# Kernel tuning notes

Measured on AMD Instinct MI355X. Metric: run time of the kernel, lower is better.

## Reference

```python
import jax, jax.numpy as jnp
import numpy as np

B, N, M, D = 2, 2048, 32, 128
H, DH = 8, 16
DI = H * DH            # dim_inner = 128
S = 5                  # 1 + max_degree + max_degree, max_degree = 2
DMLP = 256             # int(2.0 * dim_inner)


def _ln(x, g):  # LayerNorm(bias=False)
    mu = x.mean(-1, keepdims=True)
    var = ((x - mu) ** 2).mean(-1, keepdims=True)
    return (x - mu) / jnp.sqrt(var + 1e-5) * g


def _softclamp(t, v=50.0):
    return jnp.tanh(t / v) * v


def _gather(a, idx):  # a: [b, n, ...], idx: [b, i, j] -> [b, i, j, ...]
    return jax.vmap(lambda t, ix: jnp.take(t, ix, axis=0))(a, idx)


def setup_inputs():
    key = jax.random.key(0)
    ks = jax.random.split(key, 24)
    w = lambda k, i, o: jax.random.normal(k, (i, o), jnp.float32) / np.sqrt(i)
    return {
        'h': jax.random.normal(ks[0], (B, N, D), jnp.float32),
        't_ij': jax.random.normal(ks[1], (B, N, M, D), jnp.float32),
        'r_ij_1': jax.random.normal(ks[2], (B, N, M, 3), jnp.float32),
        'r_ij_2': jax.random.normal(ks[3], (B, N, M, 5), jnp.float32),
        'x_1': jax.random.normal(ks[4], (B, N, D, 3), jnp.float32),
        'x_2': jax.random.normal(ks[5], (B, N, D, 5), jnp.float32),
        'g_hi': jnp.ones((D,), jnp.float32),
        'g_hj': jnp.ones((D,), jnp.float32),
        'Wq': w(ks[6], D, DI),
        'Wk': w(ks[7], D, DI),
        'Wv1': w(ks[8], D, DMLP), 'bv1': jnp.zeros((DMLP,), jnp.float32),
        'Wv2': w(ks[9], DMLP, S * DI), 'bv2': jnp.zeros((S * DI,), jnp.float32),
        'Wp1': w(ks[10], D, DMLP), 'bp1': jnp.zeros((DMLP,), jnp.float32),
        'Wp2': w(ks[11], DMLP, S * DI), 'bp2': jnp.zeros((S * DI,), jnp.float32),
        'Wek': w(ks[12], D, S * DI),
        'Wev': w(ks[13], D, S * DI),
        'Wg': w(ks[14], D, H * S), 'bg': jnp.zeros((H * S,), jnp.float32),
        'Wc': w(ks[15], DI, D),
        'neighbor_indices': jax.random.randint(ks[16], (B, N, M), 0, N),
        'neighbor_mask': jnp.ones((B, N, M), bool),
    }


def reference(h, t_ij, r_ij_1, r_ij_2, x_1, x_2, g_hi, g_hj, Wq, Wk, Wv1, bv1,
              Wv2, bv2, Wp1, bp1, Wp2, bp2, Wek, Wev, Wg, bg, Wc,
              neighbor_indices, neighbor_mask):
    b, n, m = neighbor_indices.shape
    hi = _ln(h, g_hi)
    hj = _ln(h, g_hj)
    q = (hi @ Wq).reshape(b, n, H, DH).transpose(0, 2, 1, 3)               # b h i dh
    k = hj @ Wk                                                            # b n (h dh)
    v = jax.nn.silu(hj @ Wv1 + bv1) @ Wv2 + bv2                            # b n (s h dh)
    pav = jax.nn.silu(hj @ Wp1 + bp1) @ Wp2 + bp2                          # post-attn h values
    ek = jax.nn.silu(t_ij @ Wek)                                           # b i j (s h dh)
    ev = t_ij @ Wev
    # neighbor gathers over the node axis
    k_g = _gather(k, neighbor_indices)                                     # b i j (h dh)
    v_g = _gather(v, neighbor_indices)                                     # b i j (s h dh)
    pav_g = _gather(pav, neighbor_indices)
    heads4 = lambda t: t.reshape(b, n, m, H, DH).transpose(0, 3, 1, 2, 4)          # b h i j dh
    heads5 = lambda t: t.reshape(b, n, m, S, H, DH).transpose(0, 4, 1, 2, 3, 5)    # b h i j s dh
    keys = heads4(k_g)[..., None, :] * heads5(ek)                          # edge-fused keys
    sim = _softclamp(jnp.einsum('bhid,bhijsd->bhijs', q, keys))
    sim = jnp.where(neighbor_mask[:, None, :, :, None], sim, -jnp.finfo(sim.dtype).max)
    attn = jax.nn.softmax(sim, axis=-2)                                    # softmax over neighbors j
    sea = attn[..., None] * heads5(v_g) + heads5(ev) * heads5(pav_g)       # b h i j s dh
    gates = jax.nn.sigmoid(hi @ Wg + bg).reshape(b, n, H, S)               # layout (h s)
    sea = sea * gates.transpose(0, 2, 1, 3)[:, :, :, None, :, None]        # b h i 1 s 1
    out = sea.transpose(0, 2, 3, 4, 1, 5).reshape(b, n, m, S, DI) @ Wc     # b i j s d
    h_res = out[..., 0, :].sum(axis=2)                                     # sum over neighbors
    x_res = []
    for li, (r_l, x_l) in enumerate(((r_ij_1, x_1), (r_ij_2, x_2))):
        r_part = jnp.einsum('bijm,bijd->bidm', r_l, out[..., 1 + li, :])
        xg = _gather(x_l, neighbor_indices)                                # b i j d ml
        x_res.append(r_part + jnp.einsum('bijdm,bijd->bidm', xg, out[..., 3 + li, :]))
    return (h_res, x_res[0], x_res[1])
```

## Files before the change

kernel.cpp:

```cpp
#include <hip/hip_runtime.h>
#include <hip/hip_bf16.h>
#include <cstdint>


typedef __bf16 bf16x8 __attribute__((ext_vector_type(8)));
typedef float  f32x4  __attribute__((ext_vector_type(4)));
typedef unsigned short u16;
typedef unsigned int   u32;

__device__ __forceinline__ float sigm_(float x){ return 1.f/(1.f+__expf(-x)); }
__device__ __forceinline__ float silu_(float x){ return x/(1.f+__expf(-x)); }
__device__ __forceinline__ u16 f2b(float f){
    union{float f; u32 u;} x; x.f = f;
    u32 r = x.u + 0x7FFFu + ((x.u>>16)&1u);
    return (u16)(r>>16);
}
__device__ __forceinline__ float b2f(u16 b){
    union{u32 u; float f;} x; x.u = ((u32)b)<<16; return x.f;
}
union VecU { uint4 u; bf16x8 v; u16 s[8]; };
union Vec4 { uint2 u; u16 s[4]; };
__device__ __forceinline__ bf16x8 ld8(const u16* p){ VecU x; x.u = *(const uint4*)p; return x.v; }

__global__ __launch_bounds__(256) void prep_kernel(
    const float* __restrict__ Wek, const float* __restrict__ Wev,
    const float* __restrict__ Wc,
    const float* __restrict__ x1, const float* __restrict__ x2,
    u16* __restrict__ wekT, u16* __restrict__ wevT, u16* __restrict__ wcT,
    float* __restrict__ xT1, float* __restrict__ xT2, int do_xt)
{
    const int idx = blockIdx.x*256 + threadIdx.x;
    if (idx < 81920) {
        const int n = idx >> 7, k = idx & 127;
        wekT[idx] = f2b(Wek[k*640 + n]);
        wevT[idx] = f2b(Wev[k*640 + n]);
    }
    if (idx < 16384) {
        const int d = idx >> 7, c = idx & 127;
        wcT[idx] = f2b(Wc[c*128 + d]);
    }
    if (do_xt) {
        if (idx < 4096*384) {
            const int node = idx/384, rem = idx%384, m = rem>>7, d = rem&127;
            xT1[idx] = x1[((size_t)node*128 + d)*3 + m];
        }
        if (idx < 4096*640) {
            const int node = idx/640, rem = idx%640, m = rem>>7, d = rem&127;
            xT2[idx] = x2[((size_t)node*128 + d)*5 + m];
        }
    }
}

__global__ __launch_bounds__(256) void node_kernel(
    const float* __restrict__ h,
    const float* __restrict__ g_hi, const float* __restrict__ g_hj,
    const float* __restrict__ Wq, const float* __restrict__ Wk,
    const float* __restrict__ Wv1, const float* __restrict__ bv1,
    const float* __restrict__ Wv2, const float* __restrict__ bv2,
    const float* __restrict__ Wp1, const float* __restrict__ bp1,
    const float* __restrict__ Wp2, const float* __restrict__ bp2,
    const float* __restrict__ Wg, const float* __restrict__ bg,
    float* __restrict__ qws, float* __restrict__ kws,
    float* __restrict__ vpws, float* __restrict__ gws)
{
    const int tid  = threadIdx.x;
    const int base = blockIdx.x * 8;
    __shared__ __align__(16) float hi_s[8][128];
    __shared__ __align__(16) float hj_s[8][128];
    __shared__ __align__(16) float u_s[8][256];

    {
        const int wv = tid >> 6, lane = tid & 63;
        for (int r = wv; r < 8; r += 4) {
            const int node = base + r;
            float a  = h[node*128 + lane];
            float b2 = h[node*128 + 64 + lane];
            float s = a + b2;
            #pragma unroll
            for (int off = 32; off > 0; off >>= 1) s += __shfl_down(s, off);
            s = __shfl(s, 0);
            const float mu = s * (1.f/128.f);
            const float da = a - mu, db = b2 - mu;
            float v = da*da + db*db;
            #pragma unroll
            for (int off = 32; off > 0; off >>= 1) v += __shfl_down(v, off);
            v = __shfl(v, 0);
            const float rstd = rsqrtf(v*(1.f/128.f) + 1e-5f);
            hi_s[r][lane]    = da*rstd*g_hi[lane];
            hi_s[r][64+lane] = db*rstd*g_hi[64+lane];
            hj_s[r][lane]    = da*rstd*g_hj[lane];
            hj_s[r][64+lane] = db*rstd*g_hj[64+lane];
        }
    }
    __syncthreads();

    {
        const int o  = tid & 127;
        const int r0 = (tid >> 7) * 4;
        float aq[4], ak[4];
        #pragma unroll
        for (int r=0;r<4;r++){ aq[r]=0.f; ak[r]=0.f; }
        for (int c0=0;c0<128;c0+=4) {
            float wq0=Wq[(c0+0)*128+o], wq1=Wq[(c0+1)*128+o], wq2=Wq[(c0+2)*128+o], wq3=Wq[(c0+3)*128+o];
            float wk0=Wk[(c0+0)*128+o], wk1=Wk[(c0+1)*128+o], wk2=Wk[(c0+2)*128+o], wk3=Wk[(c0+3)*128+o];
            #pragma unroll
            for (int r=0;r<4;r++) {
                float4 hi4 = *(const float4*)(&hi_s[r0+r][c0]);
                float4 hj4 = *(const float4*)(&hj_s[r0+r][c0]);
                aq[r] += hi4.x*wq0; aq[r] += hi4.y*wq1; aq[r] += hi4.z*wq2; aq[r] += hi4.w*wq3;
                ak[r] += hj4.x*wk0; ak[r] += hj4.y*wk1; ak[r] += hj4.z*wk2; ak[r] += hj4.w*wk3;
            }
        }
        #pragma unroll
        for (int r=0;r<4;r++) {
            qws[(size_t)(base+r0+r)*128 + o] = aq[r];
            kws[(size_t)(base+r0+r)*128 + o] = ak[r];
        }
    }

    {
        const int o = tid;
        float acc[8];
        const float bias = bv1[o];
        #pragma unroll
        for (int r=0;r<8;r++) acc[r]=bias;
        for (int c0=0;c0<128;c0+=4) {
            float w0=Wv1[(c0+0)*256+o], w1=Wv1[(c0+1)*256+o], w2=Wv1[(c0+2)*256+o], w3=Wv1[(c0+3)*256+o];
            #pragma unroll
            for (int r=0;r<8;r++) {
                float4 u4 = *(const float4*)(&hj_s[r][c0]);
                acc[r] += u4.x*w0; acc[r] += u4.y*w1; acc[r] += u4.z*w2; acc[r] += u4.w*w3;
            }
        }
        #pragma unroll
        for (int r=0;r<8;r++) u_s[r][o] = silu_(acc[r]);
    }
    __syncthreads();

    for (int o=tid; o<640; o+=256) {
        float acc[8];
        const float bias = bv2[o];
        #pragma unroll
        for (int r=0;r<8;r++) acc[r]=bias;
        for (int c0=0;c0<256;c0+=4) {
            float w0=Wv2[(c0+0)*640+o], w1=Wv2[(c0+1)*640+o], w2=Wv2[(c0+2)*640+o], w3=Wv2[(c0+3)*640+o];
            #pragma unroll
            for (int r=0;r<8;r++) {
                float4 u4 = *(const float4*)(&u_s[r][c0]);
                acc[r] += u4.x*w0; acc[r] += u4.y*w1; acc[r] += u4.z*w2; acc[r] += u4.w*w3;
            }
        }
        #pragma unroll
        for (int r=0;r<8;r++)
            vpws[(size_t)(base+r)*1280 + (o>>2)*8 + (o&3)] = acc[r];
    }
    __syncthreads();

    {
        const int o = tid;
        float acc[8];
        const float bias = bp1[o];
        #pragma unroll
        for (int r=0;r<8;r++) acc[r]=bias;
        for (int c0=0;c0<128;c0+=4) {
            float w0=Wp1[(c0+0)*256+o], w1=Wp1[(c0+1)*256+o], w2=Wp1[(c0+2)*256+o], w3=Wp1[(c0+3)*256+o];
            #pragma unroll
            for (int r=0;r<8;r++) {
                float4 u4 = *(const float4*)(&hj_s[r][c0]);
                acc[r] += u4.x*w0; acc[r] += u4.y*w1; acc[r] += u4.z*w2; acc[r] += u4.w*w3;
            }
        }
        #pragma unroll
        for (int r=0;r<8;r++) u_s[r][o] = silu_(acc[r]);
    }
    __syncthreads();

    for (int o=tid; o<640; o+=256) {
        float acc[8];
        const float bias = bp2[o];
        #pragma unroll
        for (int r=0;r<8;r++) acc[r]=bias;
        for (int c0=0;c0<256;c0+=4) {
            float w0=Wp2[(c0+0)*640+o], w1=Wp2[(c0+1)*640+o], w2=Wp2[(c0+2)*640+o], w3=Wp2[(c0+3)*640+o];
            #pragma unroll
            for (int r=0;r<8;r++) {
                float4 u4 = *(const float4*)(&u_s[r][c0]);
                acc[r] += u4.x*w0; acc[r] += u4.y*w1; acc[r] += u4.z*w2; acc[r] += u4.w*w3;
            }
        }
        #pragma unroll
        for (int r=0;r<8;r++)
            vpws[(size_t)(base+r)*1280 + (o>>2)*8 + 4 + (o&3)] = acc[r];
    }

    for (int idx=tid; idx<8*40; idx+=256) {
        const int r = idx/40, hs = idx%40;
        float s = bg[hs];
        for (int c=0;c<128;c++) s += hi_s[r][c]*Wg[c*40+hs];
        gws[(size_t)(base+r)*40 + hs] = sigm_(s);
    }
}

template<bool XT>
__global__ __launch_bounds__(512,4) void edge_kernel(
    const float* __restrict__ t_ij,
    const float* __restrict__ r1, const float* __restrict__ r2,
    const float* __restrict__ x1, const float* __restrict__ x2,
    const float* __restrict__ xT1, const float* __restrict__ xT2,
    const u16* __restrict__ wekT, const u16* __restrict__ wevT,
    const u16* __restrict__ wcT,
    const int* __restrict__ nidx,
    const float* __restrict__ qws, const float* __restrict__ kws,
    const float* __restrict__ vpws,
    const float* __restrict__ gws,
    float* __restrict__ out)
{
    const int node = blockIdx.x;
    const int bN   = (node >> 11) << 11;
    const int tid  = threadIdx.x;
    const int grp  = tid >> 8;
    const int ltid = tid & 255;
    const int lane = ltid & 63, w = ltid >> 6;
    const int ll   = lane & 15, lh = lane >> 4;

    __shared__ __align__(16) u16   tj_s[32*128];
    __shared__ __align__(16) u16   chunk_s[2][80*128];
    __shared__ float sim_s[32][40];
    __shared__ __align__(16) float q_s[128];
    __shared__ float g_s[40];
    __shared__ int   jn_s[32];

    u16* chunk = chunk_s[grp];

    if (tid < 32) jn_s[tid] = nidx[node*32 + tid];
    else if (tid >= 64 && tid < 192) q_s[tid-64] = qws[(size_t)node*128 + (tid-64)];
    else if (tid >= 192 && tid < 232) g_s[tid-192] = gws[(size_t)node*40 + (tid-192)];
    __syncthreads();

    bf16x8 wcf[2][4];
    #pragma unroll
    for (int dlt=0;dlt<2;dlt++)
        #pragma unroll
        for (int ks=0;ks<4;ks++)
            wcf[dlt][ks] = ld8(wcT + (size_t)((w*2+dlt)*16 + ll)*128 + ks*32 + lh*8);

    float kq[16];
    if (ltid < 128) {
        const int j = grp*16 + (ltid >> 3), c0 = (ltid & 7) * 16;
        const float* tp = t_ij + (size_t)node*4096 + j*128 + c0;
        float4 t0 = *(const float4*)(tp+0);
        float4 t1 = *(const float4*)(tp+4);
        float4 t2 = *(const float4*)(tp+8);
        float4 t3 = *(const float4*)(tp+12);
        VecU p0, p1;
        p0.s[0]=f2b(t0.x); p0.s[1]=f2b(t0.y); p0.s[2]=f2b(t0.z); p0.s[3]=f2b(t0.w);
        p0.s[4]=f2b(t1.x); p0.s[5]=f2b(t1.y); p0.s[6]=f2b(t1.z); p0.s[7]=f2b(t1.w);
        p1.s[0]=f2b(t2.x); p1.s[1]=f2b(t2.y); p1.s[2]=f2b(t2.z); p1.s[3]=f2b(t2.w);
        p1.s[4]=f2b(t3.x); p1.s[5]=f2b(t3.y); p1.s[6]=f2b(t3.z); p1.s[7]=f2b(t3.w);
        const int el = (j*128 + c0) ^ ((j&7)<<3);
        *(uint4*)(tj_s + el)       = p0.u;
        *(uint4*)(tj_s + (el ^ 8)) = p1.u;

        const float* kp = kws + ((size_t)(bN + jn_s[j]))*128 + c0;
        #pragma unroll
        for (int i=0;i<16;i+=4) {
            float4 kv = *(const float4*)(kp+i);
            float4 qv = *(const float4*)(&q_s[c0+i]);
            kq[i+0] = qv.x*kv.x; kq[i+1] = qv.y*kv.y;
            kq[i+2] = qv.z*kv.z; kq[i+3] = qv.w*kv.w;
        }
    }
    __syncthreads();

    bf16x8 tfr[4];
    #pragma unroll
    for (int ks=0;ks<4;ks++) {
        const int j = grp*16 + ll;
        tfr[ks] = ld8(tj_s + ((j*128 + ks*32 + lh*8) ^ ((j&7)<<3)));
    }
    #pragma unroll 2
    for (int t=0;t<10;t++) {
        const int nt = w + 4*t;
        const u16* wp = wekT + (size_t)(nt*16 + ll)*128 + lh*8;
        __builtin_amdgcn_s_setprio(1);
        f32x4 aA = {0.f,0.f,0.f,0.f}, aB = {0.f,0.f,0.f,0.f};
        aA = __builtin_amdgcn_mfma_f32_16x16x32_bf16(ld8(wp +  0), tfr[0], aA, 0,0,0);
        aB = __builtin_amdgcn_mfma_f32_16x16x32_bf16(ld8(wp + 32), tfr[1], aB, 0,0,0);
        aA = __builtin_amdgcn_mfma_f32_16x16x32_bf16(ld8(wp + 64), tfr[2], aA, 0,0,0);
        aB = __builtin_amdgcn_mfma_f32_16x16x32_bf16(ld8(wp + 96), tfr[3], aB, 0,0,0);
        __builtin_amdgcn_s_setprio(0);
        f32x4 acc = aA + aB;
        const int ss = nt >> 3, c0 = (nt&7)*16 + lh*4;
        const int r  = ss*16 + ll;
        Vec4 pk;
        #pragma unroll
        for (int reg=0;reg<4;reg++) pk.s[reg] = f2b(silu_(acc[reg]));
        *(uint2*)(chunk + ((r*128 + c0) ^ ((r&7)<<3))) = pk.u;
    }
    __syncthreads();

    if (ltid < 128) {
        const int jj = ltid >> 3, hh = ltid & 7;
        #pragma unroll
        for (int ss=0; ss<5; ss++) {
            const int r = ss*16 + jj;
            const int el = (r*128 + hh*16) ^ ((r&7)<<3);
            VecU e0, e1;
            e0.u = *(const uint4*)(chunk + el);
            e1.u = *(const uint4*)(chunk + (el^8));
            float s = 0.f;
            #pragma unroll
            for (int i=0;i<8;i++) s += kq[i]   * b2f(e0.s[i]);
            #pragma unroll
            for (int i=0;i<8;i++) s += kq[8+i] * b2f(e1.s[i]);
            sim_s[grp*16 + jj][hh*5 + ss] = 50.f * tanhf(s*0.02f);
        }
    }
    __syncthreads();

    if (tid < 40) {
        float mx = -1e30f;
        #pragma unroll
        for (int j=0;j<32;j++) mx = fmaxf(mx, sim_s[j][tid]);
        float sum = 0.f;
        #pragma unroll
        for (int j=0;j<32;j++) sum += __expf(sim_s[j][tid]-mx);
        const float inv = 1.f/sum;
        #pragma unroll
        for (int j=0;j<32;j++) sim_s[j][tid] = __expf(sim_s[j][tid]-mx)*inv;
    }
    __syncthreads();

    const int edge = grp*16 + ll;
    {
        const int nj   = jn_s[edge];
        const float* vprow = vpws + (size_t)(bN + nj)*1280;

        auto body = [&](int nt, const float4& v4, const float4& pv) {
            const u16* wp = wevT + (size_t)(nt*16 + ll)*128 + lh*8;
            __builtin_amdgcn_s_setprio(1);
            f32x4 aA = {0.f,0.f,0.f,0.f}, aB = {0.f,0.f,0.f,0.f};
            aA = __builtin_amdgcn_mfma_f32_16x16x32_bf16(ld8(wp +  0), tfr[0], aA, 0,0,0);
            aB = __builtin_amdgcn_mfma_f32_16x16x32_bf16(ld8(wp + 32), tfr[1], aB, 0,0,0);
            aA = __builtin_amdgcn_mfma_f32_16x16x32_bf16(ld8(wp + 64), tfr[2], aA, 0,0,0);
            aB = __builtin_amdgcn_mfma_f32_16x16x32_bf16(ld8(wp + 96), tfr[3], aB, 0,0,0);
            __builtin_amdgcn_s_setprio(0);
            f32x4 acc = aA + aB;
            const int ss = nt >> 3, hsu = (nt&7)*5 + ss;
            const int c0 = (nt&7)*16 + lh*4;
            const float gate = g_s[hsu];
            const float attn = sim_s[edge][hsu];
            Vec4 w4;
            w4.s[0] = f2b((attn*v4.x + acc[0]*pv.x)*gate);
            w4.s[1] = f2b((attn*v4.y + acc[1]*pv.y)*gate);
            w4.s[2] = f2b((attn*v4.z + acc[2]*pv.z)*gate);
            w4.s[3] = f2b((attn*v4.w + acc[3]*pv.w)*gate);
            const int r = ss*16 + ll;
            *(uint2*)(chunk + ((r*128 + c0) ^ ((r&7)<<3))) = w4.u;
        };

        int qa = (w+0)*4 + lh, qb = (w+4)*4 + lh;
        float4 va = *(const float4*)(vprow + qa*8);
        float4 pa = *(const float4*)(vprow + qa*8 + 4);
        float4 vb = *(const float4*)(vprow + qb*8);
        float4 pb = *(const float4*)(vprow + qb*8 + 4);
        for (int tt=0; tt<5; ++tt) {
            const int nt0 = w + 8*tt, nt1 = nt0 + 4;
            const float4 v0 = va, p0 = pa, v1 = vb, p1 = pb;
            if (tt < 4) {
                const int qa2 = (nt0+8)*4 + lh, qb2 = (nt1+8)*4 + lh;
                va = *(const float4*)(vprow + qa2*8);
                pa = *(const float4*)(vprow + qa2*8 + 4);
                vb = *(const float4*)(vprow + qb2*8);
                pb = *(const float4*)(vprow + qb2*8 + 4);
            }
            body(nt0, v0, p0);
            body(nt1, v1, p1);
        }
    }
    __syncthreads();

    float accH[2] = {0,0};
    float aR1[3][2], aX1[3][2], aR2[5][2], aX2[5][2];
    #pragma unroll
    for (int m=0;m<3;m++){ aR1[m][0]=aR1[m][1]=0.f; aX1[m][0]=aX1[m][1]=0.f; }
    #pragma unroll
    for (int m=0;m<5;m++){ aR2[m][0]=aR2[m][1]=0.f; aX2[m][0]=aX2[m][1]=0.f; }

    #pragma unroll
    for (int dlt=0; dlt<2; ++dlt) {
        const int d = (w*2+dlt)*16 + ll;
        float xh1[4][3], xh2[4][5];
        #pragma unroll
        for (int reg=0;reg<4;reg++) {
            const int njg = jn_s[grp*16 + lh*4 + reg];
            if (XT) {
                const float* p1 = xT1 + ((size_t)(bN + njg)*3)*128 + d;
                const float* p2 = xT2 + ((size_t)(bN + njg)*5)*128 + d;
                #pragma unroll
                for (int m=0;m<3;m++) xh1[reg][m] = p1[m*128];
                #pragma unroll
                for (int m=0;m<5;m++) xh2[reg][m] = p2[m*128];
            } else {
                const float* p1 = x1 + ((size_t)(bN + njg)*128 + d)*3;
                const float* p2 = x2 + ((size_t)(bN + njg)*128 + d)*5;
                #pragma unroll
                for (int m=0;m<3;m++) xh1[reg][m] = p1[m];
                #pragma unroll
                for (int m=0;m<5;m++) xh2[reg][m] = p2[m];
            }
        }
        #pragma unroll 1
        for (int mt=0; mt<5; ++mt) {
            bf16x8 afr[4];
            #pragma unroll
            for (int ks=0;ks<4;ks++) {
                const int r = mt*16 + ll;
                afr[ks] = ld8(chunk + ((r*128 + ks*32 + lh*8) ^ ((r&7)<<3)));
            }
            __builtin_amdgcn_s_setprio(1);
            f32x4 dA = {0.f,0.f,0.f,0.f}, dB = {0.f,0.f,0.f,0.f};
            dA = __builtin_amdgcn_mfma_f32_16x16x32_bf16(afr[0], wcf[dlt][0], dA, 0,0,0);
            dB = __builtin_amdgcn_mfma_f32_16x16x32_bf16(afr[1], wcf[dlt][1], dB, 0,0,0);
            dA = __builtin_amdgcn_mfma_f32_16x16x32_bf16(afr[2], wcf[dlt][2], dA, 0,0,0);
            dB = __builtin_amdgcn_mfma_f32_16x16x32_bf16(afr[3], wcf[dlt][3], dB, 0,0,0);
            __builtin_amdgcn_s_setprio(0);
            f32x4 dacc = dA + dB;
            if (mt == 0) {
                accH[dlt] += dacc[0]+dacc[1]+dacc[2]+dacc[3];
            } else if (mt == 1) {
                #pragma unroll
                for (int reg=0;reg<4;reg++) {
                    const int j = grp*16 + lh*4 + reg;
                    const float* rp = r1 + ((size_t)node*32 + j)*3;
                    const float p = dacc[reg];
                    #pragma unroll
                    for (int m=0;m<3;m++) aR1[m][dlt] += rp[m]*p;
                }
            } else if (mt == 2) {
                #pragma unroll
                for (int reg=0;reg<4;reg++) {
                    const int j = grp*16 + lh*4 + reg;
                    const float* rp = r2 + ((size_t)node*32 + j)*5;
                    const float p = dacc[reg];
                    #pragma unroll
                    for (int m=0;m<5;m++) aR2[m][dlt] += rp[m]*p;
                }
            } else if (mt == 3) {
                #pragma unroll
                for (int reg=0;reg<4;reg++) {
                    const float p = dacc[reg];
                    #pragma unroll
                    for (int m=0;m<3;m++) aX1[m][dlt] += xh1[reg][m]*p;
                }
            } else {
                #pragma unroll
                for (int reg=0;reg<4;reg++) {
                    const float p = dacc[reg];
                    #pragma unroll
                    for (int m=0;m<5;m++) aX2[m][dlt] += xh2[reg][m]*p;
                }
            }
        }
    }

    #define RED2(x) { x += __shfl_xor(x,16); x += __shfl_xor(x,32); }
    #pragma unroll
    for (int dlt=0; dlt<2; ++dlt) {
        RED2(accH[dlt]);
        #pragma unroll
        for (int m=0;m<3;m++){ RED2(aR1[m][dlt]); RED2(aX1[m][dlt]); }
        #pragma unroll
        for (int m=0;m<5;m++){ RED2(aR2[m][dlt]); RED2(aX2[m][dlt]); }
    }
    __syncthreads();

    float* xch = (float*)chunk_s[0];
    if (grp == 1 && lh == 0) {
        #pragma unroll
        for (int dlt=0; dlt<2; ++dlt) {
            const int d = (w*2+dlt)*16 + ll;
            float* p = xch + d*17;
            p[0] = accH[dlt];
            #pragma unroll
            for (int m=0;m<3;m++){ p[1+m] = aR1[m][dlt]; p[4+m] = aX1[m][dlt]; }
            #pragma unroll
            for (int m=0;m<5;m++){ p[7+m] = aR2[m][dlt]; p[12+m] = aX2[m][dlt]; }
        }
    }
    __syncthreads();
    if (grp == 0 && lh == 0) {
        #pragma unroll
        for (int dlt=0; dlt<2; ++dlt) {
            const int d = (w*2+dlt)*16 + ll;
            const float* p = xch + d*17;
            out[(size_t)node*128 + d] = accH[dlt] + p[0];
            float* o1 = out + 524288 + ((size_t)node*128 + d)*3;
            #pragma unroll
            for (int m=0;m<3;m++) o1[m] = (aR1[m][dlt] + p[1+m]) + (aX1[m][dlt] + p[4+m]);
            float* o2 = out + 2097152 + ((size_t)node*128 + d)*5;
            #pragma unroll
            for (int m=0;m<5;m++) o2[m] = (aR2[m][dlt] + p[7+m]) + (aX2[m][dlt] + p[12+m]);
        }
    }
}

extern "C" void kernel_launch(void* const* d_in, const int* in_sizes, int n_in,
                              void* d_out, int out_size, void* d_ws, size_t ws_size,
                              hipStream_t stream)
{
    const float* h    = (const float*)d_in[0];
    const float* t_ij = (const float*)d_in[1];
    const float* r1   = (const float*)d_in[2];
    const float* r2   = (const float*)d_in[3];
    const float* x1   = (const float*)d_in[4];
    const float* x2   = (const float*)d_in[5];
    const float* g_hi = (const float*)d_in[6];
    const float* g_hj = (const float*)d_in[7];
    const float* Wq   = (const float*)d_in[8];
    const float* Wk   = (const float*)d_in[9];
    const float* Wv1  = (const float*)d_in[10];
    const float* bv1  = (const float*)d_in[11];
    const float* Wv2  = (const float*)d_in[12];
    const float* bv2  = (const float*)d_in[13];
    const float* Wp1  = (const float*)d_in[14];
    const float* bp1  = (const float*)d_in[15];
    const float* Wp2  = (const float*)d_in[16];
    const float* bp2  = (const float*)d_in[17];
    const float* Wek  = (const float*)d_in[18];
    const float* Wev  = (const float*)d_in[19];
    const float* Wg   = (const float*)d_in[20];
    const float* bg   = (const float*)d_in[21];
    const float* Wc   = (const float*)d_in[22];
    const int*   nidx = (const int*)d_in[23];

    char* ws = (char*)d_ws;
    float* qws   = (float*)ws;  ws += (size_t)4096*128*4;
    float* kws   = (float*)ws;  ws += (size_t)4096*128*4;
    float* gws   = (float*)ws;  ws += (size_t)4096*40*4;
    float* vpws  = (float*)ws;  ws += (size_t)4096*1280*4;
    u16*   wekT  = (u16*)ws;    ws += (size_t)81920*2;
    u16*   wevT  = (u16*)ws;    ws += (size_t)81920*2;
    u16*   wcT   = (u16*)ws;    ws += (size_t)16384*2;
    float* xT1   = (float*)ws;  ws += (size_t)4096*384*4;
    float* xT2   = (float*)ws;  ws += (size_t)4096*640*4;
    const size_t need_xt = (size_t)(ws - (char*)d_ws);
    const int use_xt = (ws_size >= need_xt) ? 1 : 0;

    hipLaunchKernelGGL(prep_kernel, dim3(use_xt ? 10240 : 320), dim3(256), 0, stream,
        Wek, Wev, Wc, x1, x2, wekT, wevT, wcT, xT1, xT2, use_xt);

    hipLaunchKernelGGL(node_kernel, dim3(512), dim3(256), 0, stream,
        h, g_hi, g_hj, Wq, Wk, Wv1, bv1, Wv2, bv2, Wp1, bp1, Wp2, bp2, Wg, bg,
        qws, kws, vpws, gws);

    if (use_xt) {
        hipLaunchKernelGGL(edge_kernel<true>, dim3(4096), dim3(512), 0, stream,
            t_ij, r1, r2, x1, x2, xT1, xT2, wekT, wevT, wcT, nidx,
            qws, kws, vpws, gws, (float*)d_out);
    } else {
        hipLaunchKernelGGL(edge_kernel<false>, dim3(4096), dim3(512), 0, stream,
            t_ij, r1, r2, x1, x2, xT1, xT2, wekT, wevT, wcT, nidx,
            qws, kws, vpws, gws, (float*)d_out);
    }
}
```

Measured before the change: 592.6 us.

## Alias t_ij tile into chunk buffer and double-buffer edge weight fragment loads

Result: slower. 1.011 ms (+70.6%).

```diff
diff --git a/kernel.cpp b/kernel.cpp
--- a/kernel.cpp
+++ b/kernel.cpp
@@ -202,7 +202,7 @@
 }
 
 template<bool XT>
-__global__ __launch_bounds__(512,4) void edge_kernel(
+__global__ __launch_bounds__(512,6) void edge_kernel(
     const float* __restrict__ t_ij,
     const float* __restrict__ r1, const float* __restrict__ r2,
     const float* __restrict__ x1, const float* __restrict__ x2,
@@ -223,7 +223,6 @@
     const int lane = ltid & 63, w = ltid >> 6;
     const int ll   = lane & 15, lh = lane >> 4;
 
-    __shared__ __align__(16) u16   tj_s[32*128];
     __shared__ __align__(16) u16   chunk_s[2][80*128];
     __shared__ float sim_s[32][40];
     __shared__ __align__(16) float q_s[128];
@@ -231,6 +230,7 @@
     __shared__ int   jn_s[32];
 
     u16* chunk = chunk_s[grp];
+    u16* tj_s  = chunk_s[0];
 
     if (tid < 32) jn_s[tid] = nidx[node*32 + tid];
     else if (tid >= 64 && tid < 192) q_s[tid-64] = qws[(size_t)node*128 + (tid-64)];
@@ -278,24 +278,40 @@
         const int j = grp*16 + ll;
         tfr[ks] = ld8(tj_s + ((j*128 + ks*32 + lh*8) ^ ((j&7)<<3)));
     }
-    #pragma unroll 2
-    for (int t=0;t<10;t++) {
-        const int nt = w + 4*t;
-        const u16* wp = wekT + (size_t)(nt*16 + ll)*128 + lh*8;
-        __builtin_amdgcn_s_setprio(1);
-        f32x4 aA = {0.f,0.f,0.f,0.f}, aB = {0.f,0.f,0.f,0.f};
-        aA = __builtin_amdgcn_mfma_f32_16x16x32_bf16(ld8(wp +  0), tfr[0], aA, 0,0,0);
-        aB = __builtin_amdgcn_mfma_f32_16x16x32_bf16(ld8(wp + 32), tfr[1], aB, 0,0,0);
-        aA = __builtin_amdgcn_mfma_f32_16x16x32_bf16(ld8(wp + 64), tfr[2], aA, 0,0,0);
-        aB = __builtin_amdgcn_mfma_f32_16x16x32_bf16(ld8(wp + 96), tfr[3], aB, 0,0,0);
-        __builtin_amdgcn_s_setprio(0);
-        f32x4 acc = aA + aB;
-        const int ss = nt >> 3, c0 = (nt&7)*16 + lh*4;
-        const int r  = ss*16 + ll;
-        Vec4 pk;
-        #pragma unroll
-        for (int reg=0;reg<4;reg++) pk.s[reg] = f2b(silu_(acc[reg]));
-        *(uint2*)(chunk + ((r*128 + c0) ^ ((r&7)<<3))) = pk.u;
+    __syncthreads();
+
+    {
+        const u16* wka = wekT + (size_t)(w*16 + ll)*128 + lh*8;
+        auto ekbody = [&](int t, bf16x8 w0, bf16x8 w1, bf16x8 w2, bf16x8 w3) {
+            const int nt = w + 4*t;
+            __builtin_amdgcn_s_setprio(1);
+            f32x4 aA = {0.f,0.f,0.f,0.f}, aB = {0.f,0.f,0.f,0.f};
+            aA = __builtin_amdgcn_mfma_f32_16x16x32_bf16(w0, tfr[0], aA, 0,0,0);
+            aB = __builtin_amdgcn_mfma_f32_16x16x32_bf16(w1, tfr[1], aB, 0,0,0);
+            aA = __builtin_amdgcn_mfma_f32_16x16x32_bf16(w2, tfr[2], aA, 0,0,0);
+            aB = __builtin_amdgcn_mfma_f32_16x16x32_bf16(w3, tfr[3], aB, 0,0,0);
+            __builtin_amdgcn_s_setprio(0);
+            f32x4 acc = aA + aB;
+            const int ss = nt >> 3, c0 = (nt&7)*16 + lh*4;
+            const int r  = ss*16 + ll;
+            Vec4 pk;
+            #pragma unroll
+            for (int reg=0;reg<4;reg++) pk.s[reg] = f2b(silu_(acc[reg]));
+            *(uint2*)(chunk + ((r*128 + c0) ^ ((r&7)<<3))) = pk.u;
+        };
+        bf16x8 fA0=ld8(wka+0), fA1=ld8(wka+32), fA2=ld8(wka+64), fA3=ld8(wka+96);
+        bf16x8 fB0, fB1, fB2, fB3;
+        #pragma unroll
+        for (int tp=0; tp<5; ++tp) {
+            const u16* pB = wka + (size_t)(2*tp+1)*8192;
+            fB0=ld8(pB+0); fB1=ld8(pB+32); fB2=ld8(pB+64); fB3=ld8(pB+96);
+            ekbody(2*tp, fA0, fA1, fA2, fA3);
+            if (tp < 4) {
+                const u16* pA = wka + (size_t)(2*tp+2)*8192;
+                fA0=ld8(pA+0); fA1=ld8(pA+32); fA2=ld8(pA+64); fA3=ld8(pA+96);
+            }
+            ekbody(2*tp+1, fB0, fB1, fB2, fB3);
+        }
     }
     __syncthreads();
 
@@ -335,15 +351,17 @@
     {
         const int nj   = jn_s[edge];
         const float* vprow = vpws + (size_t)(bN + nj)*1280;
-
-        auto body = [&](int nt, const float4& v4, const float4& pv) {
-            const u16* wp = wevT + (size_t)(nt*16 + ll)*128 + lh*8;
+        const u16* wva = wevT + (size_t)(w*16 + ll)*128 + lh*8;
+
+        auto body = [&](int t, bf16x8 w0, bf16x8 w1, bf16x8 w2, bf16x8 w3,
+                        const float4& v4, const float4& pv) {
+            const int nt = w + 4*t;
             __builtin_amdgcn_s_setprio(1);
             f32x4 aA = {0.f,0.f,0.f,0.f}, aB = {0.f,0.f,0.f,0.f};
-            aA = __builtin_amdgcn_mfma_f32_16x16x32_bf16(ld8(wp +  0), tfr[0], aA, 0,0,0);
-            aB = __builtin_amdgcn_mfma_f32_16x16x32_bf16(ld8(wp + 32), tfr[1], aB, 0,0,0);
-            aA = __builtin_amdgcn_mfma_f32_16x16x32_bf16(ld8(wp + 64), tfr[2], aA, 0,0,0);
-            aB = __builtin_amdgcn_mfma_f32_16x16x32_bf16(ld8(wp + 96), tfr[3], aB, 0,0,0);
+            aA = __builtin_amdgcn_mfma_f32_16x16x32_bf16(w0, tfr[0], aA, 0,0,0);
+            aB = __builtin_amdgcn_mfma_f32_16x16x32_bf16(w1, tfr[1], aB, 0,0,0);
+            aA = __builtin_amdgcn_mfma_f32_16x16x32_bf16(w2, tfr[2], aA, 0,0,0);
+            aB = __builtin_amdgcn_mfma_f32_16x16x32_bf16(w3, tfr[3], aB, 0,0,0);
             __builtin_amdgcn_s_setprio(0);
             f32x4 acc = aA + aB;
             const int ss = nt >> 3, hsu = (nt&7)*5 + ss;
@@ -364,18 +382,27 @@
         float4 pa = *(const float4*)(vprow + qa*8 + 4);
         float4 vb = *(const float4*)(vprow + qb*8);
         float4 pb = *(const float4*)(vprow + qb*8 + 4);
-        for (int tt=0; tt<5; ++tt) {
-            const int nt0 = w + 8*tt, nt1 = nt0 + 4;
+        bf16x8 fA0=ld8(wva+0), fA1=ld8(wva+32), fA2=ld8(wva+64), fA3=ld8(wva+96);
+        bf16x8 fB0, fB1, fB2, fB3;
+        #pragma unroll
+        for (int tp=0; tp<5; ++tp) {
+            const int t0 = 2*tp, t1 = 2*tp+1;
             const float4 v0 = va, p0 = pa, v1 = vb, p1 = pb;
-            if (tt < 4) {
-                const int qa2 = (nt0+8)*4 + lh, qb2 = (nt1+8)*4 + lh;
+            const u16* pB = wva + (size_t)t1*8192;
+            fB0=ld8(pB+0); fB1=ld8(pB+32); fB2=ld8(pB+64); fB3=ld8(pB+96);
+            if (tp < 4) {
+                const int qa2 = ((w + 4*t0)+8)*4 + lh, qb2 = ((w + 4*t1)+8)*4 + lh;
                 va = *(const float4*)(vprow + qa2*8);
                 pa = *(const float4*)(vprow + qa2*8 + 4);
                 vb = *(const float4*)(vprow + qb2*8);
                 pb = *(const float4*)(vprow + qb2*8 + 4);
             }
-            body(nt0, v0, p0);
-            body(nt1, v1, p1);
+            body(t0, fA0, fA1, fA2, fA3, v0, p0);
+            if (tp < 4) {
+                const u16* pA = wva + (size_t)(t1+1)*8192;
+                fA0=ld8(pA+0); fA1=ld8(pA+32); fA2=ld8(pA+64); fA3=ld8(pA+96);
+            }
+            body(t1, fB0, fB1, fB2, fB3, v1, p1);
         }
     }
     __syncthreads();
```
